# Optimization experiments

Measured on AMD Instinct MI355X. Metric: run time of the kernel, lower is better.

The kernel has to match this reference:

```python
import jax, jax.numpy as jnp
import numpy as np
import math

B, N, DIN, DOUT, H = 8, 1024, 256, 256, 8
HD = DOUT // H  # head_dim = 32


def setup_inputs() -> dict:
    key = jax.random.key(0)
    ks = jax.random.split(key, 12)
    x = jax.random.normal(ks[0], (B, N, DIN), dtype=jnp.float32)
    adj = jax.random.uniform(ks[1], (B, N, N), dtype=jnp.float32)
    mask = jnp.ones((B, N), dtype=bool)
    # per-head moire params: shift/width = 1.0 +- U(-0.2, 0.2), shape (1,H,1,1)
    shifts = (1.0 + jax.random.uniform(ks[2], (H,), minval=-0.2, maxval=0.2)).reshape(1, H, 1, 1).astype(jnp.float32)
    widths = (1.0 + jax.random.uniform(ks[3], (H,), minval=-0.2, maxval=0.2)).reshape(1, H, 1, 1).astype(jnp.float32)
    s_qkv = 1.0 / math.sqrt(DIN)
    Wqkv = jax.random.uniform(ks[4], (3 * DOUT, DIN), minval=-s_qkv, maxval=s_qkv, dtype=jnp.float32)
    bqkv = jax.random.uniform(ks[5], (3 * DOUT,), minval=-s_qkv, maxval=s_qkv, dtype=jnp.float32)
    s_ff = 1.0 / math.sqrt(DOUT)
    W1 = jax.random.uniform(ks[6], (DOUT, DOUT), minval=-s_ff, maxval=s_ff, dtype=jnp.float32)
    b1 = jax.random.uniform(ks[7], (DOUT,), minval=-s_ff, maxval=s_ff, dtype=jnp.float32)
    W2 = jax.random.uniform(ks[8], (DOUT, DOUT), minval=-s_ff, maxval=s_ff, dtype=jnp.float32)
    b2 = jax.random.uniform(ks[9], (DOUT,), minval=-s_ff, maxval=s_ff, dtype=jnp.float32)
    Wp = jax.random.uniform(ks[10], (DOUT, DIN), minval=-s_qkv, maxval=s_qkv, dtype=jnp.float32)
    bp = jax.random.uniform(ks[11], (DOUT,), minval=-s_qkv, maxval=s_qkv, dtype=jnp.float32)
    residual_weight = jnp.float32(0.5)
    return dict(x=x, adj=adj, mask=mask, shifts=shifts, widths=widths,
                Wqkv=Wqkv, bqkv=bqkv, W1=W1, b1=b1, W2=W2, b2=b2,
                Wp=Wp, bp=bp, residual_weight=residual_weight)


def reference(x, adj, mask, shifts, widths, Wqkv, bqkv, W1, b1, W2, b2, Wp, bp, residual_weight):
    mf = mask.astype(x.dtype)
    # fused QKV projection: (B,N,3*DOUT) -> (3,B,H,N,HD)
    qkv = (x @ Wqkv.T + bqkv).reshape(B, N, 3, H, HD)
    qkv = jnp.transpose(qkv, (2, 0, 3, 1, 4))
    Q, K, V = qkv[0], qkv[1], qkv[2]
    scores = jnp.einsum('bhnd,bhmd->bhnm', Q, K) / jnp.float32(math.sqrt(HD))
    # gaussian radial focus of adjacency, per head; clamp(min=1e-9)
    moire = jnp.exp(-((adj[:, None] - shifts) ** 2) / (2.0 * widths ** 2))
    moire = jnp.maximum(moire, 1e-9)
    adj_scores = scores * jnp.log(moire) + jnp.eye(N, dtype=x.dtype) * 0.1
    mask2d = mask[:, None, :] & mask[:, :, None]  # (B,N,N)
    adj_scores = jnp.where(mask2d[:, None], adj_scores, jnp.float32(-1000.0))
    attn = jax.nn.softmax(adj_scores, axis=-1)
    h = jnp.einsum('bhnm,bhmd->bhnd', attn, V)
    h = jnp.transpose(h, (0, 2, 1, 3)).reshape(B, N, DOUT)
    h = h * mf[..., None]
    # FFN in eval mode: noise/dropout are identity
    h = jax.nn.relu(h @ W1.T + b1) @ W2.T + b2
    h = h * mf[..., None]
    x_proj = x @ Wp.T + bp
    return residual_weight * h + (1.0 - residual_weight) * x_proj
```

## Files before the change

kernel.cpp:

```cpp
#include <hip/hip_runtime.h>
#include <math.h>

#define B_    8
#define N_    1024
#define DIN_  256
#define DOUT_ 256
#define H_    8
#define HD_   32
#define SCALE_  0.17677669529663687f
#define LOGMIN_ -20.7232658f

typedef float f32x4 __attribute__((ext_vector_type(4)));
typedef short bf16x8 __attribute__((ext_vector_type(8)));
typedef unsigned short u16;
typedef unsigned short u16x8 __attribute__((ext_vector_type(8)));

__device__ __forceinline__ u16 f2bf(float f) {
    unsigned u = __float_as_uint(f);
    u += 0x7fff + ((u >> 16) & 1);
    return (u16)(u >> 16);
}
__device__ __forceinline__ float bf2f(u16 h) {
    return __uint_as_float(((unsigned)h) << 16);
}
__device__ __forceinline__ void split_store(float v, u16* __restrict__ hi,
                                            u16* __restrict__ lo, size_t idx) {
    u16 h = f2bf(v);
    hi[idx] = h;
    lo[idx] = f2bf(v - bf2f(h));
}

#define NX_    (B_ * N_ * DIN_)
#define NWQ_   (3 * DOUT_ * DIN_)
#define NW_    (DOUT_ * DOUT_)
#define NWALL_ (NWQ_ + NW_)

__global__ __launch_bounds__(256) void prep_kernel(const float* __restrict__ x,
        const float* __restrict__ wq, const float* __restrict__ wp,
        const float* __restrict__ w1, const float* __restrict__ w2,
        u16* __restrict__ xs_h, u16* __restrict__ xs_l,
        u16* __restrict__ wall_h, u16* __restrict__ wall_l,
        u16* __restrict__ w1_h, u16* __restrict__ w1_l,
        u16* __restrict__ w2_h, u16* __restrict__ w2_l) {
    size_t i = ((size_t)blockIdx.x * 256 + threadIdx.x) * 4;
    const float* src; u16 *dh, *dl; size_t j;
    if (i < NX_)                        { src = x;  dh = xs_h;   dl = xs_l;   j = i; }
    else if (i < NX_ + NWQ_)            { src = wq; dh = wall_h; dl = wall_l; j = i - NX_; }
    else if (i < NX_ + NWALL_)          { src = wp; dh = wall_h; dl = wall_l; j = (i - NX_ - NWQ_) + NWQ_; }
    else if (i < NX_ + NWALL_ + NW_)    { src = w1; dh = w1_h;   dl = w1_l;   j = i - (NX_ + NWALL_); }
    else                                { src = w2; dh = w2_h;   dl = w2_l;   j = i - (NX_ + NWALL_ + NW_); }
    size_t sj = (dh == wall_h && j >= NWQ_) ? (j - NWQ_) : j;
    float4 v = *reinterpret_cast<const float4*>(&src[sj]);
    ushort4 hv, lv;
    hv.x = f2bf(v.x); lv.x = f2bf(v.x - bf2f(hv.x));
    hv.y = f2bf(v.y); lv.y = f2bf(v.y - bf2f(hv.y));
    hv.z = f2bf(v.z); lv.z = f2bf(v.z - bf2f(hv.z));
    hv.w = f2bf(v.w); lv.w = f2bf(v.w - bf2f(hv.w));
    *reinterpret_cast<ushort4*>(&dh[j]) = hv;
    *reinterpret_cast<ushort4*>(&dl[j]) = lv;
}

#define LDH 40

__device__ __forceinline__ void stage_pair(const u16* __restrict__ hi, const u16* __restrict__ lo,
                                           int ldk, int row0, int k0,
                                           u16 (*dh)[LDH], u16 (*dl)[LDH], int t) {
    int row = t >> 2, kk = (t & 3) << 3;
    size_t off = (size_t)(row0 + row) * ldk + k0 + kk;
    u16x8 a = *reinterpret_cast<const u16x8*>(&hi[off]);
    u16x8 b = *reinterpret_cast<const u16x8*>(&lo[off]);
    *reinterpret_cast<u16x8*>(&dh[row][kk]) = a;
    *reinterpret_cast<u16x8*>(&dl[row][kk]) = b;
}

__device__ __forceinline__ void mfma_step(u16 (*ahi)[LDH], u16 (*alo)[LDH],
                                          u16 (*bhi)[LDH], u16 (*blo)[LDH],
                                          f32x4 acc[2][2], int wr, int wc, int lane) {
    int rsel = lane & 15;
    int g8   = (lane >> 4) << 3;
    bf16x8 ah[2], al[2], bh[2], bl[2];
#pragma unroll
    for (int m = 0; m < 2; ++m) {
        int row = wr * 32 + m * 16 + rsel;
        ah[m] = *reinterpret_cast<const bf16x8*>(&ahi[row][g8]);
        al[m] = *reinterpret_cast<const bf16x8*>(&alo[row][g8]);
    }
#pragma unroll
    for (int n = 0; n < 2; ++n) {
        int col = wc * 32 + n * 16 + rsel;
        bh[n] = *reinterpret_cast<const bf16x8*>(&bhi[col][g8]);
        bl[n] = *reinterpret_cast<const bf16x8*>(&blo[col][g8]);
    }
#pragma unroll
    for (int m = 0; m < 2; ++m)
#pragma unroll
        for (int n = 0; n < 2; ++n) {
            acc[m][n] = __builtin_amdgcn_mfma_f32_16x16x32_bf16(ah[m], bh[n], acc[m][n], 0, 0, 0);
            acc[m][n] = __builtin_amdgcn_mfma_f32_16x16x32_bf16(ah[m], bl[n], acc[m][n], 0, 0, 0);
            acc[m][n] = __builtin_amdgcn_mfma_f32_16x16x32_bf16(al[m], bh[n], acc[m][n], 0, 0, 0);
        }
}

__device__ __forceinline__ void gemm_pair(const u16* Ah, const u16* Al,
                                          const u16* Bh, const u16* Bl,
                                          int K, int row0, int col0, f32x4 acc[2][2],
                                          u16 (*ah)[LDH], u16 (*al)[LDH],
                                          u16 (*bh)[LDH], u16 (*bl)[LDH],
                                          int t, int wr, int wc, int lane) {
    for (int k0 = 0; k0 < K; k0 += 32) {
        __syncthreads();
        stage_pair(Ah, Al, K, row0, k0, ah, al, t);
        stage_pair(Bh, Bl, K, col0, k0, bh, bl, t);
        __syncthreads();
        mfma_step(ah, al, bh, bl, acc, wr, wc, lane);
    }
}

__global__ __launch_bounds__(256) void proj_mfma(const u16* __restrict__ xs_h, const u16* __restrict__ xs_l,
                                                 const u16* __restrict__ wall_h, const u16* __restrict__ wall_l,
                                                 const float* __restrict__ bqkv,
                                                 const float* __restrict__ bp,
                                                 u16* __restrict__ q_h, u16* __restrict__ q_l,
                                                 u16* __restrict__ k_h, u16* __restrict__ k_l,
                                                 u16* __restrict__ vt_h, u16* __restrict__ vt_l,
                                                 float* __restrict__ xp) {
    __shared__ u16 ahi[64][LDH], alo[64][LDH], bhi[64][LDH], blo[64][LDH];
    int row0 = blockIdx.y * 64, col0 = blockIdx.x * 64;
    int t = threadIdx.x, lane = t & 63, wid = t >> 6, wr = wid >> 1, wc = wid & 1;
    f32x4 acc[2][2] = {};
    gemm_pair(xs_h, xs_l, wall_h, wall_l, DIN_, row0, col0, acc, ahi, alo, bhi, blo, t, wr, wc, lane);

    int rsel = lane & 15, rgrp = (lane >> 4) << 2;
#pragma unroll
    for (int n = 0; n < 2; ++n) {
        int col = col0 + wc * 32 + n * 16 + rsel;
        int s = col >> 8, hh = (col >> 5) & 7, hd = col & 31;
        float bv = (s < 3) ? bqkv[col] : bp[col - 768];
#pragma unroll
        for (int m = 0; m < 2; ++m)
#pragma unroll
            for (int r = 0; r < 4; ++r) {
                int row = row0 + wr * 32 + m * 16 + rgrp + r;
                int bb = row >> 10, nn = row & 1023;
                float v = acc[m][n][r] + bv;
                if (s == 0) {
                    split_store(v * SCALE_, q_h, q_l, ((size_t)(bb * H_ + hh) * N_ + nn) * HD_ + hd);
                } else if (s == 1) {
                    split_store(v, k_h, k_l, ((size_t)(bb * H_ + hh) * N_ + nn) * HD_ + hd);
                } else if (s == 2) {
                    split_store(v, vt_h, vt_l, ((size_t)(bb * H_ + hh) * HD_ + hd) * N_ + nn);
                } else {
                    xp[(size_t)row * DOUT_ + (col - 768)] = v;
                }
            }
    }
}

__global__ __launch_bounds__(512) void attn_mfma(const u16* __restrict__ qh_, const u16* __restrict__ ql_,
                                                 const u16* __restrict__ kh_, const u16* __restrict__ kl_,
                                                 const u16* __restrict__ vth_, const u16* __restrict__ vtl_,
                                                 const float* __restrict__ adj,
                                                 const float* __restrict__ shifts,
                                                 const float* __restrict__ widths,
                                                 u16* __restrict__ h_hi, u16* __restrict__ h_lo) {
    __shared__ u16 ksh[64][LDH], ksl[64][LDH];
    __shared__ u16 vsh[32][72],  vsl[32][72];
    __shared__ u16 ps[128][72];

    int bhid = blockIdx.y, bb = bhid >> 3, h = bhid & 7;
    int q0 = blockIdx.x * 128;
    int t = threadIdx.x, lane = t & 63, w = t >> 6, qsub = w << 4;
    int lr = lane & 15, g = lane >> 4;
    int qg = q0 + qsub;

    float shift = shifts[h], wd = widths[h];
    float cneg = -1.0f / (2.0f * wd * wd);

    const u16* Kh  = kh_  + (size_t)bhid * N_ * HD_;
    const u16* Kl  = kl_  + (size_t)bhid * N_ * HD_;
    const u16* Vth = vth_ + (size_t)bhid * HD_ * N_;
    const u16* Vtl = vtl_ + (size_t)bhid * HD_ * N_;
    const float* adjq = adj + (size_t)bb * N_ * N_ + (size_t)(qg + (g << 2)) * N_ + lr;

    bf16x8 qfh = *reinterpret_cast<const bf16x8*>(&qh_[((size_t)bhid * N_ + qg + lr) * HD_ + g * 8]);
    bf16x8 qfl = *reinterpret_cast<const bf16x8*>(&ql_[((size_t)bhid * N_ + qg + lr) * HD_ + g * 8]);

    f32x4 o0 = {0.f, 0.f, 0.f, 0.f}, o1 = {0.f, 0.f, 0.f, 0.f};
    float rmax[4] = {-3e38f, -3e38f, -3e38f, -3e38f};
    float rsum[4] = {0.f, 0.f, 0.f, 0.f};

    for (int m0 = 0; m0 < N_; m0 += 64) {
        __syncthreads();
        if (t < 256) {
            int srow = t >> 2, skk = (t & 3) << 3;
            size_t off = (size_t)(m0 + srow) * HD_ + skk;
            *reinterpret_cast<u16x8*>(&ksh[srow][skk]) = *reinterpret_cast<const u16x8*>(&Kh[off]);
            *reinterpret_cast<u16x8*>(&ksl[srow][skk]) = *reinterpret_cast<const u16x8*>(&Kl[off]);
        } else {
            int tv = t - 256;
            int sd = tv >> 3, sm8 = (tv & 7) << 3;
            size_t off = (size_t)sd * N_ + m0 + sm8;
            *reinterpret_cast<u16x8*>(&vsh[sd][sm8]) = *reinterpret_cast<const u16x8*>(&Vth[off]);
            *reinterpret_cast<u16x8*>(&vsl[sd][sm8]) = *reinterpret_cast<const u16x8*>(&Vtl[off]);
        }
        float adjv[4][4];
#pragma unroll
        for (int mf = 0; mf < 4; ++mf)
#pragma unroll
            for (int r = 0; r < 4; ++r)
                adjv[mf][r] = adjq[(size_t)r * N_ + m0 + mf * 16];
        __syncthreads();

        f32x4 sa[4];
#pragma unroll
        for (int mf = 0; mf < 4; ++mf) {
            bf16x8 kfh = *reinterpret_cast<const bf16x8*>(&ksh[mf * 16 + lr][g * 8]);
            bf16x8 kfl = *reinterpret_cast<const bf16x8*>(&ksl[mf * 16 + lr][g * 8]);
            f32x4 c = {0.f, 0.f, 0.f, 0.f};
            c = __builtin_amdgcn_mfma_f32_16x16x32_bf16(qfh, kfh, c, 0, 0, 0);
            c = __builtin_amdgcn_mfma_f32_16x16x32_bf16(qfh, kfl, c, 0, 0, 0);
            c = __builtin_amdgcn_mfma_f32_16x16x32_bf16(qfl, kfh, c, 0, 0, 0);
            sa[mf] = c;
        }

        bool dt = (m0 == (qg & ~63));
        int lqo = qg - m0 + (g << 2);
        float corr[4];
#pragma unroll
        for (int r = 0; r < 4; ++r) {
            float mx = -3e38f;
#pragma unroll
            for (int mf = 0; mf < 4; ++mf) {
                float a  = adjv[mf][r] - shift;
                float lm = fmaxf(a * a * cneg, LOGMIN_);
                float lg = sa[mf][r] * lm;
                if (dt && (lqo + r == mf * 16 + lr)) lg += 0.1f;
                sa[mf][r] = lg;
                mx = fmaxf(mx, lg);
            }
            mx = fmaxf(mx, __shfl_xor(mx, 1));
            mx = fmaxf(mx, __shfl_xor(mx, 2));
            mx = fmaxf(mx, __shfl_xor(mx, 4));
            mx = fmaxf(mx, __shfl_xor(mx, 8));
            float nm = fmaxf(rmax[r], mx);
            float cr = __expf(rmax[r] - nm);
            rmax[r] = nm;
            float ts = 0.f;
#pragma unroll
            for (int mf = 0; mf < 4; ++mf) {
                float p = __expf(sa[mf][r] - nm);
                sa[mf][r] = p;
                ts += p;
            }
            ts += __shfl_xor(ts, 1);
            ts += __shfl_xor(ts, 2);
            ts += __shfl_xor(ts, 4);
            ts += __shfl_xor(ts, 8);
            rsum[r] = rsum[r] * cr + ts;
            corr[r] = cr;
        }
#pragma unroll
        for (int r = 0; r < 4; ++r) { o0[r] *= corr[r]; o1[r] *= corr[r]; }

#pragma unroll
        for (int mf = 0; mf < 4; ++mf)
#pragma unroll
            for (int r = 0; r < 4; ++r)
                ps[qsub + (g << 2) + r][mf * 16 + lr] = f2bf(sa[mf][r]);

#pragma unroll
        for (int kc = 0; kc < 2; ++kc) {
            bf16x8 pa  = *reinterpret_cast<const bf16x8*>(&ps[qsub + lr][kc * 32 + g * 8]);
            bf16x8 v0h = *reinterpret_cast<const bf16x8*>(&vsh[lr][kc * 32 + g * 8]);
            bf16x8 v0l = *reinterpret_cast<const bf16x8*>(&vsl[lr][kc * 32 + g * 8]);
            bf16x8 v1h = *reinterpret_cast<const bf16x8*>(&vsh[lr + 16][kc * 32 + g * 8]);
            bf16x8 v1l = *reinterpret_cast<const bf16x8*>(&vsl[lr + 16][kc * 32 + g * 8]);
            o0 = __builtin_amdgcn_mfma_f32_16x16x32_bf16(pa, v0h, o0, 0, 0, 0);
            o0 = __builtin_amdgcn_mfma_f32_16x16x32_bf16(pa, v0l, o0, 0, 0, 0);
            o1 = __builtin_amdgcn_mfma_f32_16x16x32_bf16(pa, v1h, o1, 0, 0, 0);
            o1 = __builtin_amdgcn_mfma_f32_16x16x32_bf16(pa, v1l, o1, 0, 0, 0);
        }
    }

#pragma unroll
    for (int r = 0; r < 4; ++r) {
        float inv = 1.0f / rsum[r];
        size_t base = ((size_t)(bb * N_ + qg + (g << 2) + r)) * DOUT_ + h * HD_;
        split_store(o0[r] * inv, h_hi, h_lo, base + lr);
        split_store(o1[r] * inv, h_hi, h_lo, base + 16 + lr);
    }
}

__global__ __launch_bounds__(256) void ffn1_mfma(const u16* __restrict__ h_hi, const u16* __restrict__ h_lo,
                                                 const u16* __restrict__ w1_h, const u16* __restrict__ w1_l,
                                                 const float* __restrict__ b1,
                                                 u16* __restrict__ tb_h, u16* __restrict__ tb_l) {
    __shared__ u16 ahi[64][LDH], alo[64][LDH], bhi[64][LDH], blo[64][LDH];
    int row0 = blockIdx.y * 64, col0 = blockIdx.x * 64;
    int t = threadIdx.x, lane = t & 63, wid = t >> 6, wr = wid >> 1, wc = wid & 1;
    f32x4 acc[2][2] = {};
    gemm_pair(h_hi, h_lo, w1_h, w1_l, DOUT_, row0, col0, acc, ahi, alo, bhi, blo, t, wr, wc, lane);

    int rsel = lane & 15, rgrp = (lane >> 4) << 2;
#pragma unroll
    for (int n = 0; n < 2; ++n) {
        int col = col0 + wc * 32 + n * 16 + rsel;
        float bv = b1[col];
#pragma unroll
        for (int m = 0; m < 2; ++m)
#pragma unroll
            for (int r = 0; r < 4; ++r) {
                int row = row0 + wr * 32 + m * 16 + rgrp + r;
                split_store(fmaxf(acc[m][n][r] + bv, 0.0f), tb_h, tb_l, (size_t)row * DOUT_ + col);
            }
    }
}

__global__ __launch_bounds__(256) void final2_mfma(const u16* __restrict__ tb_h, const u16* __restrict__ tb_l,
                                                   const u16* __restrict__ w2_h, const u16* __restrict__ w2_l,
                                                   const float* __restrict__ b2,
                                                   const float* __restrict__ rw,
                                                   float* __restrict__ out) {
    __shared__ u16 ahi[64][LDH], alo[64][LDH], bhi[64][LDH], blo[64][LDH];
    int row0 = blockIdx.y * 64, col0 = blockIdx.x * 64;
    int t = threadIdx.x, lane = t & 63, wid = t >> 6, wr = wid >> 1, wc = wid & 1;
    f32x4 acc[2][2] = {};
    gemm_pair(tb_h, tb_l, w2_h, w2_l, DOUT_, row0, col0, acc, ahi, alo, bhi, blo, t, wr, wc, lane);

    int rsel = lane & 15, rgrp = (lane >> 4) << 2;
    float r_ = rw[0];
#pragma unroll
    for (int n = 0; n < 2; ++n) {
        int col = col0 + wc * 32 + n * 16 + rsel;
        float b2v = b2[col];
#pragma unroll
        for (int m = 0; m < 2; ++m)
#pragma unroll
            for (int rr = 0; rr < 4; ++rr) {
                int row = row0 + wr * 32 + m * 16 + rgrp + rr;
                size_t idx = (size_t)row * DOUT_ + col;
                float xpv = out[idx];
                out[idx] = r_ * (acc[m][n][rr] + b2v) + (1.0f - r_) * xpv;
            }
    }
}

extern "C" void kernel_launch(void* const* d_in, const int* in_sizes, int n_in,
                              void* d_out, int out_size, void* d_ws, size_t ws_size,
                              hipStream_t stream) {
    const float* x      = (const float*)d_in[0];
    const float* adj    = (const float*)d_in[1];
    const float* shifts = (const float*)d_in[3];
    const float* widths = (const float*)d_in[4];
    const float* Wqkv   = (const float*)d_in[5];
    const float* bqkv   = (const float*)d_in[6];
    const float* W1     = (const float*)d_in[7];
    const float* b1     = (const float*)d_in[8];
    const float* W2     = (const float*)d_in[9];
    const float* b2     = (const float*)d_in[10];
    const float* Wp     = (const float*)d_in[11];
    const float* bp     = (const float*)d_in[12];
    const float* rw     = (const float*)d_in[13];
    float* out = (float*)d_out;

    u16* p = (u16*)d_ws;
    u16* xs_h   = p;          p += NX_;
    u16* xs_l   = p;          p += NX_;
    u16* wall_h = p;          p += NWALL_;
    u16* wall_l = p;          p += NWALL_;
    u16* w1_h   = p;          p += NW_;
    u16* w1_l   = p;          p += NW_;
    u16* w2_h   = p;          p += NW_;
    u16* w2_l   = p;          p += NW_;
    u16* q_h    = p;          p += NX_;
    u16* q_l    = p;          p += NX_;
    u16* k_h    = p;          p += NX_;
    u16* k_l    = p;          p += NX_;
    u16* vt_h   = p;          p += NX_;
    u16* vt_l   = p;          p += NX_;
    u16* h_hi   = p;          p += NX_;
    u16* h_lo   = p;          p += NX_;
    u16* tb_h   = p;          p += NX_;
    u16* tb_l   = p;          p += NX_;

    prep_kernel<<<(NX_ + NWALL_ + 2 * NW_) / 4 / 256, 256, 0, stream>>>(
        x, Wqkv, Wp, W1, W2, xs_h, xs_l, wall_h, wall_l, w1_h, w1_l, w2_h, w2_l);
    proj_mfma<<<dim3(1024 / 64, B_ * N_ / 64), 256, 0, stream>>>(
        xs_h, xs_l, wall_h, wall_l, bqkv, bp, q_h, q_l, k_h, k_l, vt_h, vt_l, out);
    attn_mfma<<<dim3(N_ / 128, B_ * H_), 512, 0, stream>>>(
        q_h, q_l, k_h, k_l, vt_h, vt_l, adj, shifts, widths, h_hi, h_lo);
    ffn1_mfma<<<dim3(DOUT_ / 64, B_ * N_ / 64), 256, 0, stream>>>(
        h_hi, h_lo, w1_h, w1_l, b1, tb_h, tb_l);
    final2_mfma<<<dim3(DOUT_ / 64, B_ * N_ / 64), 256, 0, stream>>>(
        tb_h, tb_l, w2_h, w2_l, b2, rw, out);
}
```

Before: 238.3 us.

## Store V row-major with in-LDS transpose and halve FFN GEMM row tiles

The projection kernel now writes V in the same row-major [bh][n][hd] layout as K instead of a transposed layout. This replaces strided scattered global stores with contiguous ones. The attention kernel transposes V while staging it into LDS, using scalar stores that may cause bank conflicts. The FFN GEMMs switch from 64x64 to 32x64 tiles, doubling the block count for better occupancy at the cost of less reuse per block.

```diff
diff --git a/kernel.cpp b/kernel.cpp
--- a/kernel.cpp
+++ b/kernel.cpp
@@ -101,34 +101,25 @@
         }
 }
 
-__device__ __forceinline__ void gemm_pair(const u16* Ah, const u16* Al,
-                                          const u16* Bh, const u16* Bl,
-                                          int K, int row0, int col0, f32x4 acc[2][2],
-                                          u16 (*ah)[LDH], u16 (*al)[LDH],
-                                          u16 (*bh)[LDH], u16 (*bl)[LDH],
-                                          int t, int wr, int wc, int lane) {
-    for (int k0 = 0; k0 < K; k0 += 32) {
-        __syncthreads();
-        stage_pair(Ah, Al, K, row0, k0, ah, al, t);
-        stage_pair(Bh, Bl, K, col0, k0, bh, bl, t);
-        __syncthreads();
-        mfma_step(ah, al, bh, bl, acc, wr, wc, lane);
-    }
-}
-
 __global__ __launch_bounds__(256) void proj_mfma(const u16* __restrict__ xs_h, const u16* __restrict__ xs_l,
                                                  const u16* __restrict__ wall_h, const u16* __restrict__ wall_l,
                                                  const float* __restrict__ bqkv,
                                                  const float* __restrict__ bp,
                                                  u16* __restrict__ q_h, u16* __restrict__ q_l,
                                                  u16* __restrict__ k_h, u16* __restrict__ k_l,
-                                                 u16* __restrict__ vt_h, u16* __restrict__ vt_l,
+                                                 u16* __restrict__ v_h, u16* __restrict__ v_l,
                                                  float* __restrict__ xp) {
     __shared__ u16 ahi[64][LDH], alo[64][LDH], bhi[64][LDH], blo[64][LDH];
     int row0 = blockIdx.y * 64, col0 = blockIdx.x * 64;
     int t = threadIdx.x, lane = t & 63, wid = t >> 6, wr = wid >> 1, wc = wid & 1;
     f32x4 acc[2][2] = {};
-    gemm_pair(xs_h, xs_l, wall_h, wall_l, DIN_, row0, col0, acc, ahi, alo, bhi, blo, t, wr, wc, lane);
+    for (int k0 = 0; k0 < DIN_; k0 += 32) {
+        __syncthreads();
+        stage_pair(xs_h, xs_l, DIN_, row0, k0, ahi, alo, t);
+        stage_pair(wall_h, wall_l, DIN_, col0, k0, bhi, blo, t);
+        __syncthreads();
+        mfma_step(ahi, alo, bhi, blo, acc, wr, wc, lane);
+    }
 
     int rsel = lane & 15, rgrp = (lane >> 4) << 2;
 #pragma unroll
@@ -148,7 +139,7 @@
                 } else if (s == 1) {
                     split_store(v, k_h, k_l, ((size_t)(bb * H_ + hh) * N_ + nn) * HD_ + hd);
                 } else if (s == 2) {
-                    split_store(v, vt_h, vt_l, ((size_t)(bb * H_ + hh) * HD_ + hd) * N_ + nn);
+                    split_store(v, v_h, v_l, ((size_t)(bb * H_ + hh) * N_ + nn) * HD_ + hd);
                 } else {
                     xp[(size_t)row * DOUT_ + (col - 768)] = v;
                 }
@@ -158,7 +149,7 @@
 
 __global__ __launch_bounds__(512) void attn_mfma(const u16* __restrict__ qh_, const u16* __restrict__ ql_,
                                                  const u16* __restrict__ kh_, const u16* __restrict__ kl_,
-                                                 const u16* __restrict__ vth_, const u16* __restrict__ vtl_,
+                                                 const u16* __restrict__ vh_, const u16* __restrict__ vl_,
                                                  const float* __restrict__ adj,
                                                  const float* __restrict__ shifts,
                                                  const float* __restrict__ widths,
@@ -176,10 +167,10 @@
     float shift = shifts[h], wd = widths[h];
     float cneg = -1.0f / (2.0f * wd * wd);
 
-    const u16* Kh  = kh_  + (size_t)bhid * N_ * HD_;
-    const u16* Kl  = kl_  + (size_t)bhid * N_ * HD_;
-    const u16* Vth = vth_ + (size_t)bhid * HD_ * N_;
-    const u16* Vtl = vtl_ + (size_t)bhid * HD_ * N_;
+    const u16* Kh = kh_ + (size_t)bhid * N_ * HD_;
+    const u16* Kl = kl_ + (size_t)bhid * N_ * HD_;
+    const u16* Vh = vh_ + (size_t)bhid * N_ * HD_;
+    const u16* Vl = vl_ + (size_t)bhid * N_ * HD_;
     const float* adjq = adj + (size_t)bb * N_ * N_ + (size_t)(qg + (g << 2)) * N_ + lr;
 
     bf16x8 qfh = *reinterpret_cast<const bf16x8*>(&qh_[((size_t)bhid * N_ + qg + lr) * HD_ + g * 8]);
@@ -198,10 +189,15 @@
             *reinterpret_cast<u16x8*>(&ksl[srow][skk]) = *reinterpret_cast<const u16x8*>(&Kl[off]);
         } else {
             int tv = t - 256;
-            int sd = tv >> 3, sm8 = (tv & 7) << 3;
-            size_t off = (size_t)sd * N_ + m0 + sm8;
-            *reinterpret_cast<u16x8*>(&vsh[sd][sm8]) = *reinterpret_cast<const u16x8*>(&Vth[off]);
-            *reinterpret_cast<u16x8*>(&vsl[sd][sm8]) = *reinterpret_cast<const u16x8*>(&Vtl[off]);
+            int vrow = tv >> 2, d8 = (tv & 3) << 3;
+            size_t off = (size_t)(m0 + vrow) * HD_ + d8;
+            u16x8 a = *reinterpret_cast<const u16x8*>(&Vh[off]);
+            u16x8 b = *reinterpret_cast<const u16x8*>(&Vl[off]);
+#pragma unroll
+            for (int j = 0; j < 8; ++j) {
+                vsh[d8 + j][vrow] = a[j];
+                vsl[d8 + j][vrow] = b[j];
+            }
         }
         float adjv[4][4];
 #pragma unroll
@@ -291,28 +287,65 @@
     }
 }
 
+__device__ __forceinline__ void stage_AB32(const u16* __restrict__ Ah, const u16* __restrict__ Al, int row0,
+                                           const u16* __restrict__ Bh, const u16* __restrict__ Bl, int col0,
+                                           int ldk, int k0,
+                                           u16 (*ah)[LDH], u16 (*al)[LDH],
+                                           u16 (*bh)[LDH], u16 (*bl)[LDH], int t) {
+    int row = t >> 2, kk = (t & 3) << 3;
+    size_t boff = (size_t)(col0 + row) * ldk + k0 + kk;
+    *reinterpret_cast<u16x8*>(&bh[row][kk]) = *reinterpret_cast<const u16x8*>(&Bh[boff]);
+    *reinterpret_cast<u16x8*>(&bl[row][kk]) = *reinterpret_cast<const u16x8*>(&Bl[boff]);
+    if (t < 128) {
+        size_t aoff = (size_t)(row0 + row) * ldk + k0 + kk;
+        *reinterpret_cast<u16x8*>(&ah[row][kk]) = *reinterpret_cast<const u16x8*>(&Ah[aoff]);
+        *reinterpret_cast<u16x8*>(&al[row][kk]) = *reinterpret_cast<const u16x8*>(&Al[aoff]);
+    }
+}
+
+__device__ __forceinline__ void mfma_step32(u16 (*ahi)[LDH], u16 (*alo)[LDH],
+                                            u16 (*bhi)[LDH], u16 (*blo)[LDH],
+                                            f32x4 acc[2], int wr, int wc, int lane) {
+    int rsel = lane & 15;
+    int g8   = (lane >> 4) << 3;
+    int row  = wr * 16 + rsel;
+    bf16x8 ah = *reinterpret_cast<const bf16x8*>(&ahi[row][g8]);
+    bf16x8 al = *reinterpret_cast<const bf16x8*>(&alo[row][g8]);
+#pragma unroll
+    for (int n = 0; n < 2; ++n) {
+        int col = wc * 32 + n * 16 + rsel;
+        bf16x8 bh = *reinterpret_cast<const bf16x8*>(&bhi[col][g8]);
+        bf16x8 bl = *reinterpret_cast<const bf16x8*>(&blo[col][g8]);
+        acc[n] = __builtin_amdgcn_mfma_f32_16x16x32_bf16(ah, bh, acc[n], 0, 0, 0);
+        acc[n] = __builtin_amdgcn_mfma_f32_16x16x32_bf16(ah, bl, acc[n], 0, 0, 0);
+        acc[n] = __builtin_amdgcn_mfma_f32_16x16x32_bf16(al, bh, acc[n], 0, 0, 0);
+    }
+}
+
 __global__ __launch_bounds__(256) void ffn1_mfma(const u16* __restrict__ h_hi, const u16* __restrict__ h_lo,
                                                  const u16* __restrict__ w1_h, const u16* __restrict__ w1_l,
                                                  const float* __restrict__ b1,
                                                  u16* __restrict__ tb_h, u16* __restrict__ tb_l) {
-    __shared__ u16 ahi[64][LDH], alo[64][LDH], bhi[64][LDH], blo[64][LDH];
-    int row0 = blockIdx.y * 64, col0 = blockIdx.x * 64;
+    __shared__ u16 ahi[32][LDH], alo[32][LDH], bhi[64][LDH], blo[64][LDH];
+    int row0 = blockIdx.y * 32, col0 = blockIdx.x * 64;
     int t = threadIdx.x, lane = t & 63, wid = t >> 6, wr = wid >> 1, wc = wid & 1;
-    f32x4 acc[2][2] = {};
-    gemm_pair(h_hi, h_lo, w1_h, w1_l, DOUT_, row0, col0, acc, ahi, alo, bhi, blo, t, wr, wc, lane);
-
+    f32x4 acc[2] = {};
+    for (int k0 = 0; k0 < DOUT_; k0 += 32) {
+        __syncthreads();
+        stage_AB32(h_hi, h_lo, row0, w1_h, w1_l, col0, DOUT_, k0, ahi, alo, bhi, blo, t);
+        __syncthreads();
+        mfma_step32(ahi, alo, bhi, blo, acc, wr, wc, lane);
+    }
     int rsel = lane & 15, rgrp = (lane >> 4) << 2;
 #pragma unroll
     for (int n = 0; n < 2; ++n) {
         int col = col0 + wc * 32 + n * 16 + rsel;
         float bv = b1[col];
 #pragma unroll
-        for (int m = 0; m < 2; ++m)
-#pragma unroll
-            for (int r = 0; r < 4; ++r) {
-                int row = row0 + wr * 32 + m * 16 + rgrp + r;
-                split_store(fmaxf(acc[m][n][r] + bv, 0.0f), tb_h, tb_l, (size_t)row * DOUT_ + col);
-            }
+        for (int r = 0; r < 4; ++r) {
+            int row = row0 + wr * 16 + rgrp + r;
+            split_store(fmaxf(acc[n][r] + bv, 0.0f), tb_h, tb_l, (size_t)row * DOUT_ + col);
+        }
     }
 }
 
@@ -321,12 +354,16 @@
                                                    const float* __restrict__ b2,
                                                    const float* __restrict__ rw,
                                                    float* __restrict__ out) {
-    __shared__ u16 ahi[64][LDH], alo[64][LDH], bhi[64][LDH], blo[64][LDH];
-    int row0 = blockIdx.y * 64, col0 = blockIdx.x * 64;
+    __shared__ u16 ahi[32][LDH], alo[32][LDH], bhi[64][LDH], blo[64][LDH];
+    int row0 = blockIdx.y * 32, col0 = blockIdx.x * 64;
     int t = threadIdx.x, lane = t & 63, wid = t >> 6, wr = wid >> 1, wc = wid & 1;
-    f32x4 acc[2][2] = {};
-    gemm_pair(tb_h, tb_l, w2_h, w2_l, DOUT_, row0, col0, acc, ahi, alo, bhi, blo, t, wr, wc, lane);
-
+    f32x4 acc[2] = {};
+    for (int k0 = 0; k0 < DOUT_; k0 += 32) {
+        __syncthreads();
+        stage_AB32(tb_h, tb_l, row0, w2_h, w2_l, col0, DOUT_, k0, ahi, alo, bhi, blo, t);
+        __syncthreads();
+        mfma_step32(ahi, alo, bhi, blo, acc, wr, wc, lane);
+    }
     int rsel = lane & 15, rgrp = (lane >> 4) << 2;
     float r_ = rw[0];
 #pragma unroll
@@ -334,14 +371,12 @@
         int col = col0 + wc * 32 + n * 16 + rsel;
         float b2v = b2[col];
 #pragma unroll
-        for (int m = 0; m < 2; ++m)
-#pragma unroll
-            for (int rr = 0; rr < 4; ++rr) {
-                int row = row0 + wr * 32 + m * 16 + rgrp + rr;
-                size_t idx = (size_t)row * DOUT_ + col;
-                float xpv = out[idx];
-                out[idx] = r_ * (acc[m][n][rr] + b2v) + (1.0f - r_) * xpv;
-            }
+        for (int rr = 0; rr < 4; ++rr) {
+            int row = row0 + wr * 16 + rgrp + rr;
+            size_t idx = (size_t)row * DOUT_ + col;
+            float xpv = out[idx];
+            out[idx] = r_ * (acc[n][rr] + b2v) + (1.0f - r_) * xpv;
+        }
     }
 }
 
@@ -376,8 +411,8 @@
     u16* q_l    = p;          p += NX_;
     u16* k_h    = p;          p += NX_;
     u16* k_l    = p;          p += NX_;
-    u16* vt_h   = p;          p += NX_;
-    u16* vt_l   = p;          p += NX_;
+    u16* v_h    = p;          p += NX_;
+    u16* v_l    = p;          p += NX_;
     u16* h_hi   = p;          p += NX_;
     u16* h_lo   = p;          p += NX_;
     u16* tb_h   = p;          p += NX_;
@@ -386,11 +421,11 @@
     prep_kernel<<<(NX_ + NWALL_ + 2 * NW_) / 4 / 256, 256, 0, stream>>>(
         x, Wqkv, Wp, W1, W2, xs_h, xs_l, wall_h, wall_l, w1_h, w1_l, w2_h, w2_l);
     proj_mfma<<<dim3(1024 / 64, B_ * N_ / 64), 256, 0, stream>>>(
-        xs_h, xs_l, wall_h, wall_l, bqkv, bp, q_h, q_l, k_h, k_l, vt_h, vt_l, out);
+        xs_h, xs_l, wall_h, wall_l, bqkv, bp, q_h, q_l, k_h, k_l, v_h, v_l, out);
     attn_mfma<<<dim3(N_ / 128, B_ * H_), 512, 0, stream>>>(
-        q_h, q_l, k_h, k_l, vt_h, vt_l, adj, shifts, widths, h_hi, h_lo);
-    ffn1_mfma<<<dim3(DOUT_ / 64, B_ * N_ / 64), 256, 0, stream>>>(
+        q_h, q_l, k_h, k_l, v_h, v_l, adj, shifts, widths, h_hi, h_lo);
+    ffn1_mfma<<<dim3(DOUT_ / 64, B_ * N_ / 32), 256, 0, stream>>>(
         h_hi, h_lo, w1_h, w1_l, b1, tb_h, tb_l);
-    final2_mfma<<<dim3(DOUT_ / 64, B_ * N_ / 64), 256, 0, stream>>>(
+    final2_mfma<<<dim3(DOUT_ / 64, B_ * N_ / 32), 256, 0, stream>>>(
         tb_h, tb_l, w2_h, w2_l, b2, rw, out);
 }
```

New measurement: 219.9 us. 7.7% less time.
